# Optimization experiments

Measured on AMD Instinct MI355X. Metric: run time of the kernel, lower is better.

Reference implementation:

```python
import jax, jax.numpy as jnp
import numpy as np

B, S, D, H = 2, 2048, 768, 12
DH = D // H


def setup_inputs() -> dict:
    key = jax.random.key(0)
    ks = jax.random.split(key, 12)
    f32 = jnp.float32
    sd = 1.0 / np.sqrt(D)
    return {
        "q": jax.random.normal(ks[0], (B, S, D), f32),
        "k": jax.random.normal(ks[1], (B, S, D), f32),
        "v": jax.random.normal(ks[2], (B, S, D), f32),
        "mask": jax.random.normal(ks[3], (S, S), f32),
        "Wq": jax.random.normal(ks[4], (D, D), f32) * sd,
        "bq": jnp.zeros((D,), f32),
        "Wk": jax.random.normal(ks[5], (D, D), f32) * sd,
        "bk": jnp.zeros((D,), f32),
        "Wv": jax.random.normal(ks[6], (D, D), f32) * sd,
        "bv": jnp.zeros((D,), f32),
        "Wo": jax.random.normal(ks[7], (D, D), f32) * sd,
        "bo": jnp.zeros((D,), f32),
    }


def reference(q, k, v, mask, Wq, bq, Wk, bk, Wv, bv, Wo, bo):
    # torch nn.Linear: y = x @ W.T + b
    qh = (q @ Wq.T + bq).reshape(B, S, H, DH).transpose(0, 2, 1, 3)  # [B,H,S,DH]
    kh = (k @ Wk.T + bk).reshape(B, S, H, DH).transpose(0, 2, 1, 3)
    vh = (v @ Wv.T + bv).reshape(B, S, H, DH).transpose(0, 2, 1, 3)
    scores = jnp.einsum("bhsd,bhtd->bhst", qh, kh)  # [B,H,S,S]
    # original adds mask after permute to [H,B,S,S]; with an [S,S] mask the
    # broadcast add is identical either way
    scores = scores + mask
    attn = jax.nn.softmax(scores.astype(jnp.float32) / np.sqrt(DH), axis=-1)
    out = jnp.einsum("bhst,bhtd->bhsd", attn, vh)  # [B,H,S,DH]
    out = out.transpose(0, 2, 1, 3).reshape(B, S, D)
    return out @ Wo.T + bo
```

## Files before the change

kernel.cpp:

```cpp
#include <hip/hip_runtime.h>
#include <hip/hip_bf16.h>

#define B_ 2
#define S_ 2048
#define D_ 768
#define H_ 12
#define DH_ 64
#define M_ (B_*S_)
#define BH_ (B_*H_)

typedef __bf16 v8bf __attribute__((ext_vector_type(8)));
typedef __bf16 v4bf __attribute__((ext_vector_type(4)));
typedef float  v4f  __attribute__((ext_vector_type(4)));

static __device__ __forceinline__ v4f mfma16(v8bf a, v8bf b, v4f c) {
  return __builtin_amdgcn_mfma_f32_16x16x32_bf16(a, b, c, 0, 0, 0);
}

static __device__ __forceinline__ void gload_lds16(const __bf16* g, __bf16* l) {
  __builtin_amdgcn_global_load_lds(
      (const __attribute__((address_space(1))) unsigned int*)g,
      (__attribute__((address_space(3))) unsigned int*)l,
      16, 0, 0);
}

#define C1_ 0.18033688011112042f

__global__ __launch_bounds__(256) void convert_kernel(
    const float* __restrict__ q, const float* __restrict__ k, const float* __restrict__ v,
    const float* __restrict__ Wq, const float* __restrict__ Wk,
    const float* __restrict__ Wv, const float* __restrict__ Wo,
    __bf16* __restrict__ Xq, __bf16* __restrict__ Xk, __bf16* __restrict__ Xv,
    __bf16* __restrict__ Wqb, __bf16* __restrict__ Wkb,
    __bf16* __restrict__ Wvb, __bf16* __restrict__ Wob)
{
  const float* src; __bf16* dst; int n;
  switch (blockIdx.y) {
    case 0: src = q;  dst = Xq;  n = M_*D_; break;
    case 1: src = k;  dst = Xk;  n = M_*D_; break;
    case 2: src = v;  dst = Xv;  n = M_*D_; break;
    case 3: src = Wq; dst = Wqb; n = D_*D_; break;
    case 4: src = Wk; dst = Wkb; n = D_*D_; break;
    case 5: src = Wv; dst = Wvb; n = D_*D_; break;
    default: src = Wo; dst = Wob; n = D_*D_; break;
  }
  int n4 = n >> 2;
  for (int i = blockIdx.x*blockDim.x + threadIdx.x; i < n4; i += gridDim.x*blockDim.x) {
    float4 x = ((const float4*)src)[i];
    v4bf y;
    y[0] = (__bf16)x.x; y[1] = (__bf16)x.y; y[2] = (__bf16)x.z; y[3] = (__bf16)x.w;
    ((v4bf*)dst)[i] = y;
  }
}

__global__ __launch_bounds__(256) void em_kernel(
    const float* __restrict__ mask, __bf16* __restrict__ em)
{
  int t = blockIdx.x*256 + threadIdx.x;
  int L = t & 63; int rest = t >> 6;
  int w = rest & 7; rest >>= 3;
  int kt = rest & 63; rest >>= 6;
  int qt = rest;
  int row = qt*128 + w*16 + (L & 15);
  int key0 = kt*32 + ((L >> 4) << 2);
  const float* mp = mask + (size_t)row*S_ + key0;
  float4 m0 = *(const float4*)mp;
  float4 m1 = *(const float4*)(mp + 16);
  v8bf e;
  e[0] = (__bf16)exp2f(C1_*m0.x); e[1] = (__bf16)exp2f(C1_*m0.y);
  e[2] = (__bf16)exp2f(C1_*m0.z); e[3] = (__bf16)exp2f(C1_*m0.w);
  e[4] = (__bf16)exp2f(C1_*m1.x); e[5] = (__bf16)exp2f(C1_*m1.y);
  e[6] = (__bf16)exp2f(C1_*m1.z); e[7] = (__bf16)exp2f(C1_*m1.w);
  *(v8bf*)(em + (size_t)t*8) = e;
}

template<int BM, int BN>
static __device__ __forceinline__ void gemm_core_lds(
    const __bf16* __restrict__ A, const __bf16* __restrict__ W,
    int m0, int n0, __bf16* lds, v4f acc[BM/32][BN/32])
{
  constexpr int NFA = BM/16, NFB = BN/16;
  constexpr int PW  = (NFA + NFB) / 4;
  constexpr int MI  = BM/32, NJ = BN/32;
  const int lane = threadIdx.x & 63;
  const int wave = threadIdx.x >> 6;
  const int r16 = lane & 15;
  const int kc8 = (lane >> 4) << 3;
  const int ia = (wave >> 1) * MI;
  const int ib = (wave & 1) * NJ;

  const __bf16* gsrc[PW]; __bf16* ldst[PW];
  #pragma unroll
  for (int t = 0; t < PW; t++) {
    int fb = wave*PW + t;
    gsrc[t] = (fb < NFA)
        ? A + (size_t)(m0 + fb*16 + r16)*D_ + kc8
        : W + (size_t)(n0 + (fb - NFA)*16 + r16)*D_ + kc8;
    ldst[t] = lds + fb*512;
  }

  for (int k0 = 0; k0 < D_; k0 += 32) {
    #pragma unroll
    for (int t = 0; t < PW; t++) gload_lds16(gsrc[t] + k0, ldst[t]);
    __syncthreads();
    v8bf a[MI], b[NJ];
    #pragma unroll
    for (int i = 0; i < MI; i++) a[i] = *(const v8bf*)(lds + (ia+i)*512 + lane*8);
    #pragma unroll
    for (int j = 0; j < NJ; j++) b[j] = *(const v8bf*)(lds + (NFA+ib+j)*512 + lane*8);
    #pragma unroll
    for (int i = 0; i < MI; i++)
      #pragma unroll
      for (int j = 0; j < NJ; j++)
        acc[i][j] = mfma16(a[i], b[j], acc[i][j]);
    __syncthreads();
  }
}

__global__ __launch_bounds__(256) void qkv_gemm(
    const __bf16* __restrict__ Xq, const __bf16* __restrict__ Xk, const __bf16* __restrict__ Xv,
    const __bf16* __restrict__ Wqb, const __bf16* __restrict__ Wkb, const __bf16* __restrict__ Wvb,
    const float* __restrict__ bq, const float* __restrict__ bk, const float* __restrict__ bv,
    __bf16* __restrict__ qf, __bf16* __restrict__ kf, __bf16* __restrict__ vf)
{
  __shared__ __bf16 lds[(128+64)*32];
  const int mode = blockIdx.z;
  const __bf16* A = (mode == 0) ? Xq : (mode == 1) ? Xk : Xv;
  const __bf16* W = (mode == 0) ? Wqb : (mode == 1) ? Wkb : Wvb;
  const float* bias = (mode == 0) ? bq : (mode == 1) ? bk : bv;
  const int m0 = blockIdx.y << 7, n0 = blockIdx.x << 6;
  v4f acc[4][2];
  #pragma unroll
  for (int i = 0; i < 4; i++)
    #pragma unroll
    for (int j = 0; j < 2; j++) { v4f z = {0.f,0.f,0.f,0.f}; acc[i][j] = z; }
  gemm_core_lds<128,64>(A, W, m0, n0, lds, acc);

  const int lane = threadIdx.x & 63;
  const int wave = threadIdx.x >> 6;
  const int wm = (wave >> 1) << 6, wn = (wave & 1) << 5;
  const int col = lane & 15, quad = lane >> 4;
  float bb[2]; int nn[2];
  #pragma unroll
  for (int j = 0; j < 2; j++) { nn[j] = n0 + wn + 16*j + col; bb[j] = bias[nn[j]]; }

  if (mode < 2) {
    __bf16* dst = (mode == 0) ? qf : kf;
    const float sc = (mode == 0) ? C1_ : 1.0f;
    #pragma unroll
    for (int i = 0; i < 4; i++)
      #pragma unroll
      for (int r = 0; r < 4; r++) {
        int m = m0 + wm + 16*i + quad*4 + r;
        int batch = m >> 11, s = m & (S_-1);
        #pragma unroll
        for (int j = 0; j < 2; j++) {
          int n = nn[j];
          int h = n >> 6, dd = n & 63;
          size_t flat = (((size_t)(batch*H_ + h)*128 + (s >> 4))*2 + (dd >> 5))*512
                      + ((((dd >> 3) & 3)*16 + (s & 15)) << 3) + (dd & 7);
          dst[flat] = (__bf16)((acc[i][j][r] + bb[j]) * sc);
        }
      }
  } else {
    #pragma unroll
    for (int i = 0; i < 4; i++) {
      int mbase = m0 + wm + 16*i + quad*4;
      int batch = mbase >> 11, s0 = mbase & (S_-1);
      #pragma unroll
      for (int j = 0; j < 2; j++) {
        int n = nn[j];
        int h = n >> 6, dd = n & 63;
        v4bf pk;
        #pragma unroll
        for (int r = 0; r < 4; r++) pk[r] = (__bf16)(acc[i][j][r] + bb[j]);
        size_t flat = (((size_t)(batch*H_ + h)*64 + (s0 >> 5))*4 + (dd >> 4))*512
                    + ((((s0 >> 3) & 3)*16 + (dd & 15)) << 3) + (s0 & 7);
        *(v4bf*)(vf + flat) = pk;
      }
    }
  }
}

__global__ __launch_bounds__(512, 4) void attn_kernel(
    const __bf16* __restrict__ qf, const __bf16* __restrict__ kf, const __bf16* __restrict__ vf,
    const __bf16* __restrict__ em, __bf16* __restrict__ ao)
{
  __shared__ __bf16 kv[2][2][2048];
  __shared__ __bf16 plds[8][16][40];

  const int bh = blockIdx.y;
  const int qt = blockIdx.x;
  const int wave = threadIdx.x >> 6, lane = threadIdx.x & 63;
  const int col = lane & 15, quad = lane >> 4, koff = quad << 3;
  const int batch = bh / H_, h = bh % H_;
  const __bf16* qfb = qf + (size_t)bh * (S_*DH_);
  const __bf16* kfb = kf + (size_t)bh * (S_*DH_);
  const __bf16* vfb = vf + (size_t)bh * (S_*DH_);
  const __bf16* emb = em + (size_t)qt * 262144 + wave*512;
  __bf16 (*pt)[40] = plds[wave];

  const __bf16* qblk = qfb + (size_t)(qt*8 + wave)*1024;
  v8bf Qf0 = *(const v8bf*)(qblk + lane*8);
  v8bf Qf1 = *(const v8bf*)(qblk + 512 + lane*8);

  v4f O[4];
  #pragma unroll
  for (int f = 0; f < 4; f++) { v4f z = {0.f,0.f,0.f,0.f}; O[f] = z; }
  float li = 0.f;

  const __bf16* gsrc = ((wave < 4) ? kfb : vfb) + ((wave & 3) << 9) + lane*8;
  __bf16* ld0 = &kv[0][wave >> 2][(wave & 3) << 9];
  __bf16* ld1 = &kv[1][wave >> 2][(wave & 3) << 9];

  gload_lds16(gsrc, ld0);
  __syncthreads();

  #pragma unroll 2
  for (int kt = 0; kt < 64; kt++) {
    const int buf = kt & 1;
    if (kt + 1 < 64)
      gload_lds16(gsrc + (size_t)(kt + 1)*2048, buf ? ld0 : ld1);

    const __bf16* Kb = kv[buf][0];
    const __bf16* Vb = kv[buf][1];

    v8bf ef = *(const v8bf*)(emb + kt*4096 + lane*8);
    v8bf Vf0 = *(const v8bf*)(Vb + lane*8);
    v8bf Vf1 = *(const v8bf*)(Vb + 512 + lane*8);
    v8bf Vf2 = *(const v8bf*)(Vb + 1024 + lane*8);
    v8bf Vf3 = *(const v8bf*)(Vb + 1536 + lane*8);
    v8bf Ka0 = *(const v8bf*)(Kb + lane*8);
    v8bf Ka1 = *(const v8bf*)(Kb + 512 + lane*8);
    v8bf Ka2 = *(const v8bf*)(Kb + 1024 + lane*8);
    v8bf Ka3 = *(const v8bf*)(Kb + 1536 + lane*8);

    v4f s0 = {0.f,0.f,0.f,0.f}, s1 = {0.f,0.f,0.f,0.f};
    s0 = mfma16(Ka0, Qf0, s0); s0 = mfma16(Ka1, Qf1, s0);
    s1 = mfma16(Ka2, Qf0, s1); s1 = mfma16(Ka3, Qf1, s1);

    float p[8], rs = 0.f;
    #pragma unroll
    for (int j = 0; j < 4; j++) {
      p[j]   = exp2f(s0[j]) * (float)ef[j];
      p[4+j] = exp2f(s1[j]) * (float)ef[4+j];
    }
    #pragma unroll
    for (int j = 0; j < 8; j++) rs += p[j];
    li += rs;

    v4bf pk0, pk1;
    #pragma unroll
    for (int r = 0; r < 4; r++) { pk0[r] = (__bf16)p[r]; pk1[r] = (__bf16)p[4+r]; }
    *(v4bf*)(&pt[col][quad*4])      = pk0;
    *(v4bf*)(&pt[col][16 + quad*4]) = pk1;
    v8bf Pf = *(const v8bf*)(&pt[col][koff]);

    O[0] = mfma16(Vf0, Pf, O[0]);
    O[1] = mfma16(Vf1, Pf, O[1]);
    O[2] = mfma16(Vf2, Pf, O[2]);
    O[3] = mfma16(Vf3, Pf, O[3]);

    __syncthreads();
  }

  float rs = li;
  rs += __shfl_xor(rs, 16);
  rs += __shfl_xor(rs, 32);
  float invl = 1.f / rs;
  const int qg = (qt << 7) + (wave << 4) + col;
  __bf16* orow = ao + ((size_t)batch*S_ + qg)*D_ + h*DH_ + quad*4;
  #pragma unroll
  for (int f = 0; f < 4; f++) {
    v4bf o;
    #pragma unroll
    for (int r = 0; r < 4; r++) o[r] = (__bf16)(O[f][r] * invl);
    *(v4bf*)(orow + f*16) = o;
  }
}

__global__ __launch_bounds__(256) void out_gemm(
    const __bf16* __restrict__ Ao, const __bf16* __restrict__ Wob,
    const float* __restrict__ bo, float* __restrict__ out)
{
  __shared__ __bf16 lds[(64+64)*32];
  const int m0 = blockIdx.y << 6, n0 = blockIdx.x << 6;
  v4f acc[2][2];
  #pragma unroll
  for (int i = 0; i < 2; i++)
    #pragma unroll
    for (int j = 0; j < 2; j++) { v4f z = {0.f,0.f,0.f,0.f}; acc[i][j] = z; }
  gemm_core_lds<64,64>(Ao, Wob, m0, n0, lds, acc);

  const int lane = threadIdx.x & 63;
  const int wave = threadIdx.x >> 6;
  const int wm = (wave >> 1) << 5, wn = (wave & 1) << 5;
  const int col = lane & 15, quad = lane >> 4;
  float bb[2]; int nn[2];
  #pragma unroll
  for (int j = 0; j < 2; j++) { nn[j] = n0 + wn + 16*j + col; bb[j] = bo[nn[j]]; }
  #pragma unroll
  for (int i = 0; i < 2; i++)
    #pragma unroll
    for (int r = 0; r < 4; r++) {
      int m = m0 + wm + 16*i + quad*4 + r;
      #pragma unroll
      for (int j = 0; j < 2; j++)
        out[(size_t)m*D_ + nn[j]] = acc[i][j][r] + bb[j];
    }
}

extern "C" void kernel_launch(void* const* d_in, const int* in_sizes, int n_in,
                              void* d_out, int out_size, void* d_ws, size_t ws_size,
                              hipStream_t stream)
{
  const float* q    = (const float*)d_in[0];
  const float* k    = (const float*)d_in[1];
  const float* v    = (const float*)d_in[2];
  const float* mask = (const float*)d_in[3];
  const float* Wq   = (const float*)d_in[4];
  const float* bq   = (const float*)d_in[5];
  const float* Wk   = (const float*)d_in[6];
  const float* bk   = (const float*)d_in[7];
  const float* Wv   = (const float*)d_in[8];
  const float* bv   = (const float*)d_in[9];
  const float* Wo   = (const float*)d_in[10];
  const float* bo   = (const float*)d_in[11];

  const size_t XN = (size_t)M_ * D_;
  const size_t WN = (size_t)D_ * D_;
  const size_t HN = (size_t)BH_ * S_ * DH_;

  char* ws = (char*)d_ws;
  __bf16* Xq  = (__bf16*)ws;                 ws += XN * 2;
  __bf16* Xk  = (__bf16*)ws;                 ws += XN * 2;
  __bf16* Xv  = (__bf16*)ws;                 ws += XN * 2;
  __bf16* Wqb = (__bf16*)ws;                 ws += WN * 2;
  __bf16* Wkb = (__bf16*)ws;                 ws += WN * 2;
  __bf16* Wvb = (__bf16*)ws;                 ws += WN * 2;
  __bf16* Wob = (__bf16*)ws;                 ws += WN * 2;
  __bf16* qfb = (__bf16*)ws;                 ws += HN * 2;
  __bf16* kfb = (__bf16*)ws;                 ws += HN * 2;
  __bf16* vfb = (__bf16*)ws;                 ws += HN * 2;
  __bf16* aob = (__bf16*)ws;                 ws += XN * 2;
  __bf16* emb = Xq;

  convert_kernel<<<dim3(3072, 7), 256, 0, stream>>>(
      q, k, v, Wq, Wk, Wv, Wo, Xq, Xk, Xv, Wqb, Wkb, Wvb, Wob);
  qkv_gemm<<<dim3(12, 32, 3), 256, 0, stream>>>(
      Xq, Xk, Xv, Wqb, Wkb, Wvb, bq, bk, bv, qfb, kfb, vfb);
  em_kernel<<<dim3(2048), 256, 0, stream>>>(mask, emb);
  attn_kernel<<<dim3(16, 24), 512, 0, stream>>>(qfb, kfb, vfb, emb, aob);
  out_gemm<<<dim3(12, 64), 256, 0, stream>>>(aob, Wob, bo, (float*)d_out);
}
```

Before: 259.2 us.

## Deepen attention K/V pipeline to four LDS buffers with explicit vmcnt waits

Replaces the double-buffered K/V loop with a four-slot LDS ring whose loads run two tiles ahead, together with register-prefetched mask fragments. The loop is unrolled by four and uses explicit s_waitcnt vmcnt plus raw s_barrier instead of __syncthreads. The aim is to hide global load latency for K/V and the mask. In exchange it doubles the K/V LDS footprint and relaxes launch bounds to 2 waves-per-EU minimum, which can lower occupancy but leaves more registers per thread.

Measured after the change: 253.1 us. -2.3%, faster.

```diff
diff --git a/kernel.cpp b/kernel.cpp
--- a/kernel.cpp
+++ b/kernel.cpp
@@ -182,11 +182,11 @@
   }
 }
 
-__global__ __launch_bounds__(512, 4) void attn_kernel(
+__global__ __launch_bounds__(512, 2) void attn_kernel(
     const __bf16* __restrict__ qf, const __bf16* __restrict__ kf, const __bf16* __restrict__ vf,
     const __bf16* __restrict__ em, __bf16* __restrict__ ao)
 {
-  __shared__ __bf16 kv[2][2][2048];
+  __shared__ __bf16 kv[4][2][2048];
   __shared__ __bf16 plds[8][16][40];
 
   const int bh = blockIdx.y;
@@ -197,8 +197,13 @@
   const __bf16* qfb = qf + (size_t)bh * (S_*DH_);
   const __bf16* kfb = kf + (size_t)bh * (S_*DH_);
   const __bf16* vfb = vf + (size_t)bh * (S_*DH_);
-  const __bf16* emb = em + (size_t)qt * 262144 + wave*512;
+  const __bf16* emw = em + (size_t)qt * 262144 + wave*512 + lane*8;
   __bf16 (*pt)[40] = plds[wave];
+
+  const __bf16* gsrc = ((wave < 4) ? kfb : vfb) + ((wave & 3) << 9) + lane*8;
+  __bf16* kvd[4];
+  #pragma unroll
+  for (int b = 0; b < 4; b++) kvd[b] = &kv[b][wave >> 2][(wave & 3) << 9];
 
   const __bf16* qblk = qfb + (size_t)(qt*8 + wave)*1024;
   v8bf Qf0 = *(const v8bf*)(qblk + lane*8);
@@ -209,60 +214,73 @@
   for (int f = 0; f < 4; f++) { v4f z = {0.f,0.f,0.f,0.f}; O[f] = z; }
   float li = 0.f;
 
-  const __bf16* gsrc = ((wave < 4) ? kfb : vfb) + ((wave & 3) << 9) + lane*8;
-  __bf16* ld0 = &kv[0][wave >> 2][(wave & 3) << 9];
-  __bf16* ld1 = &kv[1][wave >> 2][(wave & 3) << 9];
-
-  gload_lds16(gsrc, ld0);
-  __syncthreads();
-
-  #pragma unroll 2
-  for (int kt = 0; kt < 64; kt++) {
-    const int buf = kt & 1;
-    if (kt + 1 < 64)
-      gload_lds16(gsrc + (size_t)(kt + 1)*2048, buf ? ld0 : ld1);
-
-    const __bf16* Kb = kv[buf][0];
-    const __bf16* Vb = kv[buf][1];
-
-    v8bf ef = *(const v8bf*)(emb + kt*4096 + lane*8);
-    v8bf Vf0 = *(const v8bf*)(Vb + lane*8);
-    v8bf Vf1 = *(const v8bf*)(Vb + 512 + lane*8);
-    v8bf Vf2 = *(const v8bf*)(Vb + 1024 + lane*8);
-    v8bf Vf3 = *(const v8bf*)(Vb + 1536 + lane*8);
-    v8bf Ka0 = *(const v8bf*)(Kb + lane*8);
-    v8bf Ka1 = *(const v8bf*)(Kb + 512 + lane*8);
-    v8bf Ka2 = *(const v8bf*)(Kb + 1024 + lane*8);
-    v8bf Ka3 = *(const v8bf*)(Kb + 1536 + lane*8);
-
-    v4f s0 = {0.f,0.f,0.f,0.f}, s1 = {0.f,0.f,0.f,0.f};
-    s0 = mfma16(Ka0, Qf0, s0); s0 = mfma16(Ka1, Qf1, s0);
-    s1 = mfma16(Ka2, Qf0, s1); s1 = mfma16(Ka3, Qf1, s1);
-
-    float p[8], rs = 0.f;
-    #pragma unroll
-    for (int j = 0; j < 4; j++) {
-      p[j]   = exp2f(s0[j]) * (float)ef[j];
-      p[4+j] = exp2f(s1[j]) * (float)ef[4+j];
-    }
-    #pragma unroll
-    for (int j = 0; j < 8; j++) rs += p[j];
-    li += rs;
-
-    v4bf pk0, pk1;
-    #pragma unroll
-    for (int r = 0; r < 4; r++) { pk0[r] = (__bf16)p[r]; pk1[r] = (__bf16)p[4+r]; }
-    *(v4bf*)(&pt[col][quad*4])      = pk0;
-    *(v4bf*)(&pt[col][16 + quad*4]) = pk1;
-    v8bf Pf = *(const v8bf*)(&pt[col][koff]);
-
-    O[0] = mfma16(Vf0, Pf, O[0]);
-    O[1] = mfma16(Vf1, Pf, O[1]);
-    O[2] = mfma16(Vf2, Pf, O[2]);
-    O[3] = mfma16(Vf3, Pf, O[3]);
-
-    __syncthreads();
-  }
+  asm volatile("" ::: "memory");
+  gload_lds16(gsrc, kvd[0]);
+  v8bf ef0 = *(const v8bf*)(emw);
+  asm volatile("" ::: "memory");
+  gload_lds16(gsrc + 2048, kvd[1]);
+  v8bf ef1 = *(const v8bf*)(emw + 4096);
+  v8bf ef2, ef3;
+
+#define ATT_STEP(P, EFC, EFN, ISSUE, WSTR) \
+  { \
+    asm volatile("s_waitcnt vmcnt(" WSTR ")" ::: "memory"); \
+    __builtin_amdgcn_s_barrier(); \
+    asm volatile("" ::: "memory"); \
+    if (ISSUE) { \
+      const int nkt = kt0 + (P) + 2; \
+      gload_lds16(gsrc + (size_t)nkt*2048, kvd[((P)+2)&3]); \
+      EFN = *(const v8bf*)(emw + (size_t)nkt*4096); \
+    } \
+    const __bf16* Kb = kv[(P)&3][0]; \
+    const __bf16* Vb = kv[(P)&3][1]; \
+    v8bf Ka0 = *(const v8bf*)(Kb + lane*8); \
+    v8bf Ka1 = *(const v8bf*)(Kb + 512 + lane*8); \
+    v8bf Ka2 = *(const v8bf*)(Kb + 1024 + lane*8); \
+    v8bf Ka3 = *(const v8bf*)(Kb + 1536 + lane*8); \
+    v4f s0 = {0.f,0.f,0.f,0.f}, s1 = {0.f,0.f,0.f,0.f}; \
+    s0 = mfma16(Ka0, Qf0, s0); s0 = mfma16(Ka1, Qf1, s0); \
+    s1 = mfma16(Ka2, Qf0, s1); s1 = mfma16(Ka3, Qf1, s1); \
+    float p[8], rs = 0.f; \
+    _Pragma("unroll") \
+    for (int j = 0; j < 4; j++) { \
+      p[j]   = exp2f(s0[j]) * (float)EFC[j]; \
+      p[4+j] = exp2f(s1[j]) * (float)EFC[4+j]; \
+    } \
+    _Pragma("unroll") \
+    for (int j = 0; j < 8; j++) rs += p[j]; \
+    li += rs; \
+    v4bf pk0, pk1; \
+    _Pragma("unroll") \
+    for (int r = 0; r < 4; r++) { pk0[r] = (__bf16)p[r]; pk1[r] = (__bf16)p[4+r]; } \
+    *(v4bf*)(&pt[col][quad*4])      = pk0; \
+    *(v4bf*)(&pt[col][16 + quad*4]) = pk1; \
+    v8bf Pf = *(const v8bf*)(&pt[col][koff]); \
+    v8bf Vf0 = *(const v8bf*)(Vb + lane*8); \
+    v8bf Vf1 = *(const v8bf*)(Vb + 512 + lane*8); \
+    v8bf Vf2 = *(const v8bf*)(Vb + 1024 + lane*8); \
+    v8bf Vf3 = *(const v8bf*)(Vb + 1536 + lane*8); \
+    O[0] = mfma16(Vf0, Pf, O[0]); \
+    O[1] = mfma16(Vf1, Pf, O[1]); \
+    O[2] = mfma16(Vf2, Pf, O[2]); \
+    O[3] = mfma16(Vf3, Pf, O[3]); \
+  }
+
+  #pragma unroll 1
+  for (int kt0 = 0; kt0 < 60; kt0 += 4) {
+    ATT_STEP(0, ef0, ef2, true, "2");
+    ATT_STEP(1, ef1, ef3, true, "2");
+    ATT_STEP(2, ef2, ef0, true, "2");
+    ATT_STEP(3, ef3, ef1, true, "2");
+  }
+  {
+    const int kt0 = 60;
+    ATT_STEP(0, ef0, ef2, true,  "2");
+    ATT_STEP(1, ef1, ef3, true,  "2");
+    ATT_STEP(2, ef2, ef0, false, "2");
+    ATT_STEP(3, ef3, ef1, false, "0");
+  }
+#undef ATT_STEP
 
   float rs = li;
   rs += __shfl_xor(rs, 16);
```
